# Optimization experiments

Hardware: AMD Instinct MI355X
Metric: run time of the kernel (lower is better)

## Reference

```python
import jax, jax.numpy as jnp
import numpy as np

N, L, V, H = 64, 2048, 32000, 512

def setup_inputs() -> dict:
    key = jax.random.key(0)
    ks = jax.random.split(key, 6)
    s = 1.0 / np.sqrt(H)
    return {
        "X": jax.random.randint(ks[0], (N, L), 0, V),
        "emb": jax.random.normal(ks[1], (V, H), jnp.float32),
        "W_hh": jax.random.normal(ks[2], (H, H), jnp.float32) * s,
        "b_hh": jax.random.normal(ks[3], (H,), jnp.float32) * s,
        "W_xh": jax.random.normal(ks[4], (H, H), jnp.float32) * s,
        "b_xh": jax.random.normal(ks[5], (H,), jnp.float32) * s,
    }

def reference(X, emb, W_hh, b_hh, W_xh, b_xh):
    # Embed all timesteps and apply the input projection once (batched GEMM);
    # identical math to per-step W_xh(E_t) + b_xh.
    E = emb[X]                                   # (N, L, H)
    Xh = jnp.einsum('nlh,kh->nlk', E, W_xh) + b_xh  # (N, L, H)

    def step(h, xh_t):
        # h_t = tanh(W_hh h_{t-1} + b_hh + W_xh x_t + b_xh)
        h = jnp.tanh(h @ W_hh.T + b_hh + xh_t)
        return h, h

    h0 = jnp.zeros((X.shape[0], W_hh.shape[0]), dtype=emb.dtype)
    _, H_all = jax.lax.scan(step, h0, jnp.swapaxes(Xh, 0, 1))  # (L, N, H)
    return jnp.swapaxes(H_all, 0, 1)             # (N, L, H)
```

## Files before the change

kernel.cpp:

```cpp
#include <hip/hip_runtime.h>


typedef _Float16 half8 __attribute__((ext_vector_type(8)));
typedef float    f32x4 __attribute__((ext_vector_type(4)));

#define MFMA_F16(A,B,C) __builtin_amdgcn_mfma_f32_16x16x32_f16(A,B,C,0,0,0)

static __device__ __forceinline__ half8 cvt8(const float* p){
  const f32x4* q = (const f32x4*)p;
  f32x4 a = q[0], b = q[1];
  half8 r;
  r[0]=(_Float16)a[0]; r[1]=(_Float16)a[1]; r[2]=(_Float16)a[2]; r[3]=(_Float16)a[3];
  r[4]=(_Float16)b[0]; r[5]=(_Float16)b[1]; r[6]=(_Float16)b[2]; r[7]=(_Float16)b[3];
  return r;
}

static __device__ __forceinline__ float tanh_fast(float z){
  float e = __expf(2.0f*z);
  return 1.0f - 2.0f/(e + 1.0f);
}

__global__ __launch_bounds__(256) void k_xh(
    const int* __restrict__ X, const float* __restrict__ emb,
    const float* __restrict__ Wxh, const float* __restrict__ bxh,
    const float* __restrict__ bhh, float* __restrict__ out)
{
  const int bid = blockIdx.x;
  const int bm = bid >> 3;
  const int bn = bid & 7;
  const int tid = threadIdx.x;
  const int w  = tid >> 6;
  const int l  = tid & 63;
  const int lr = l & 15, lq = l >> 4;

  const int mbase = bm*64 + (w>>1)*32;
  const int nbase = bn*64 + (w&1)*32;

  const int tok0 = X[mbase + lr];
  const int tok1 = X[mbase + 16 + lr];
  const int c0 = nbase + lr;
  const int c1 = nbase + 16 + lr;
  const float bs0 = bxh[c0] + bhh[c0];
  const float bs1 = bxh[c1] + bhh[c1];

  const float* a0 = emb + (long long)tok0*512 + lq*8;
  const float* a1 = emb + (long long)tok1*512 + lq*8;
  const float* b0 = Wxh + (long long)c0*512 + lq*8;
  const float* b1 = Wxh + (long long)c1*512 + lq*8;

  f32x4 acc00 = {0,0,0,0}, acc01 = {0,0,0,0}, acc10 = {0,0,0,0}, acc11 = {0,0,0,0};

  #pragma unroll
  for (int ks=0; ks<16; ++ks){
    half8 A0 = cvt8(a0 + ks*32);
    half8 A1 = cvt8(a1 + ks*32);
    half8 B0 = cvt8(b0 + ks*32);
    half8 B1 = cvt8(b1 + ks*32);
    acc00 = MFMA_F16(A0, B0, acc00);
    acc01 = MFMA_F16(A0, B1, acc01);
    acc10 = MFMA_F16(A1, B0, acc10);
    acc11 = MFMA_F16(A1, B1, acc11);
  }
  #pragma unroll
  for (int r=0; r<4; ++r){
    const long long m0 = mbase + 4*lq + r;
    const long long m1 = m0 + 16;
    out[m0*512 + c0] = acc00[r] + bs0;
    out[m0*512 + c1] = acc01[r] + bs1;
    out[m1*512 + c0] = acc10[r] + bs0;
    out[m1*512 + c1] = acc11[r] + bs1;
  }
}

__global__ __launch_bounds__(512, 2) void k_rnn(
    const float* __restrict__ Whh,
    float* out,
    unsigned long long* mb,
    unsigned int* flags)
{
  const int b = blockIdx.x;
  const int side    = (b>>3)&1;
  const int pair    = (b&7)*4 + (b>>4);
  const int partner = b ^ 8;
  const int tid = threadIdx.x;
  const int w = tid >> 6;
  const int l = tid & 63;
  const int lr = l & 15, lq = l >> 4;
  const int ln = l & 1;

  __shared__ _Float16 hl[2][2][264];

  for (int i = tid; i < 2*2*264; i += 512) (&hl[0][0][0])[i] = (_Float16)0.0f;

  const int cA = side*256 + w*32 + lr;
  const int cB = cA + 16;
  half8 WfA[16], WfB[16];
  #pragma unroll
  for (int ks=0; ks<8; ++ks){
    const int kown = (side*8 + ks)*32 + lq*8;
    const int kpar = ((side^1)*8 + ks)*32 + lq*8;
    WfA[ks]   = cvt8(Whh + (long long)cA*512 + kown);
    WfB[ks]   = cvt8(Whh + (long long)cB*512 + kown);
    WfA[8+ks] = cvt8(Whh + (long long)cA*512 + kpar);
    WfB[8+ks] = cvt8(Whh + (long long)cB*512 + kpar);
  }
  __syncthreads();

  const int n_row = pair*2 + ln;
  const long long row_base = (long long)n_row * 2048 * 512;
  const int ccol = side*256 + w*32 + lq*4;
  unsigned long long* mb_me = mb + (long long)b*256;
  unsigned long long* mb_pt = mb + (long long)partner*256;

  for (int t=0; t<2048; ++t){
    const int bufc = t & 1, bufp = bufc ^ 1;

    f32x4 xh0 = {0,0,0,0}, xh1 = {0,0,0,0};
    long long obase = 0;
    if (lr < 2){
      obase = row_base + (long long)t*512 + ccol;
      xh0 = *(const f32x4*)(out + obase);
      xh1 = *(const f32x4*)(out + obase + 16);
    }

    f32x4 acc0 = {0,0,0,0}, acc1 = {0,0,0,0};

    #pragma unroll
    for (int ks=0; ks<8; ++ks){
      half8 hf = *(const half8*)(&hl[bufp][ln][ks*32 + lq*8]);
      acc0 = MFMA_F16(WfA[ks], hf, acc0);
      acc1 = MFMA_F16(WfB[ks], hf, acc1);
    }

    if (t > 0){
      {
        int spin = 0;
        while (__hip_atomic_load(&flags[partner], __ATOMIC_RELAXED, __HIP_MEMORY_SCOPE_AGENT)
                 < (unsigned)t && ++spin < (1<<20)) {}
      }
      unsigned long long* mp = mb_pt + (long long)bufp*128 + ln*64;
      #pragma unroll
      for (int ks=0; ks<8; ++ks){
        const int ui = ks*8 + lq*2;
        unsigned long long u0 = __hip_atomic_load(&mp[ui],   __ATOMIC_RELAXED, __HIP_MEMORY_SCOPE_AGENT);
        unsigned long long u1 = __hip_atomic_load(&mp[ui+1], __ATOMIC_RELAXED, __HIP_MEMORY_SCOPE_AGENT);
        union { unsigned long long u[2]; half8 v; } cv;
        cv.u[0] = u0; cv.u[1] = u1;
        acc0 = MFMA_F16(WfA[8+ks], cv.v, acc0);
        acc1 = MFMA_F16(WfB[8+ks], cv.v, acc1);
      }
    }

    if (lr < 2){
      f32x4 h0, h1;
      #pragma unroll
      for (int r=0; r<4; ++r){
        h0[r] = tanh_fast(acc0[r] + xh0[r]);
        h1[r] = tanh_fast(acc1[r] + xh1[r]);
      }
      *(f32x4*)(out + obase)      = h0;
      *(f32x4*)(out + obase + 16) = h1;
      union { _Float16 h[4]; unsigned long long u; } p0, p1;
      #pragma unroll
      for (int r=0; r<4; ++r){ p0.h[r] = (_Float16)h0[r]; p1.h[r] = (_Float16)h1[r]; }
      const int cl = w*32 + lq*4;
      *(unsigned long long*)(&hl[bufc][ln][cl])      = p0.u;
      *(unsigned long long*)(&hl[bufc][ln][cl + 16]) = p1.u;
      unsigned long long* mm = mb_me + (long long)bufc*128 + ln*64;
      __hip_atomic_store(&mm[cl>>2],       p0.u, __ATOMIC_RELAXED, __HIP_MEMORY_SCOPE_AGENT);
      __hip_atomic_store(&mm[(cl>>2) + 4], p1.u, __ATOMIC_RELAXED, __HIP_MEMORY_SCOPE_AGENT);
    }

    __syncthreads();
    if (tid == 0)
      __hip_atomic_store(&flags[b], (unsigned)(t+1), __ATOMIC_RELAXED, __HIP_MEMORY_SCOPE_AGENT);
  }
}

extern "C" void kernel_launch(void* const* d_in, const int* in_sizes, int n_in,
                              void* d_out, int out_size, void* d_ws, size_t ws_size,
                              hipStream_t stream)
{
  const int*   X    = (const int*)  d_in[0];
  const float* emb  = (const float*)d_in[1];
  const float* Whh  = (const float*)d_in[2];
  const float* bhh  = (const float*)d_in[3];
  const float* Wxh  = (const float*)d_in[4];
  const float* bxh  = (const float*)d_in[5];
  float* out = (float*)d_out;

  unsigned long long* mb   = (unsigned long long*)d_ws;
  unsigned int*       flags = (unsigned int*)((char*)d_ws + 64*2048);

  hipMemsetAsync(flags, 0, 64*sizeof(unsigned int), stream);
  hipLaunchKernelGGL(k_xh,  dim3(16384), dim3(256), 0, stream, X, emb, Wxh, bxh, bhh, out);
  hipLaunchKernelGGL(k_rnn, dim3(64),    dim3(512), 0, stream, Whh, out, mb, flags);
}
```

Baseline: 8.174 ms.

## Keep whole W_hh per block, drop cross-block partner exchange in RNN

```diff
diff --git a/kernel.cpp b/kernel.cpp
--- a/kernel.cpp
+++ b/kernel.cpp
@@ -74,106 +74,93 @@
 
 __global__ __launch_bounds__(512, 2) void k_rnn(
     const float* __restrict__ Whh,
-    float* out,
-    unsigned long long* mb,
-    unsigned int* flags)
+    float* __restrict__ out)
 {
-  const int b = blockIdx.x;
-  const int side    = (b>>3)&1;
-  const int pair    = (b&7)*4 + (b>>4);
-  const int partner = b ^ 8;
+  const int b   = blockIdx.x;
   const int tid = threadIdx.x;
-  const int w = tid >> 6;
-  const int l = tid & 63;
-  const int lr = l & 15, lq = l >> 4;
-  const int ln = l & 1;
+  const int w   = tid >> 6;
+  const int l   = tid & 63;
+  const int lr  = l & 15;
+  const int kg  = l >> 4;
+  const int wc0 = w * 64;
 
-  __shared__ _Float16 hl[2][2][264];
+  __shared__ _Float16 wlds[8][16][512];
+  __shared__ _Float16 hbuf[2][2][520];
 
-  for (int i = tid; i < 2*2*264; i += 512) (&hl[0][0][0])[i] = (_Float16)0.0f;
+  for (int i = tid; i < 2*2*520; i += 512) (&hbuf[0][0][0])[i] = (_Float16)0.0f;
 
-  const int cA = side*256 + w*32 + lr;
-  const int cB = cA + 16;
-  half8 WfA[16], WfB[16];
+  half8 Wv[3][16];
   #pragma unroll
-  for (int ks=0; ks<8; ++ks){
-    const int kown = (side*8 + ks)*32 + lq*8;
-    const int kpar = ((side^1)*8 + ks)*32 + lq*8;
-    WfA[ks]   = cvt8(Whh + (long long)cA*512 + kown);
-    WfB[ks]   = cvt8(Whh + (long long)cB*512 + kown);
-    WfA[8+ks] = cvt8(Whh + (long long)cA*512 + kpar);
-    WfB[8+ks] = cvt8(Whh + (long long)cB*512 + kpar);
+  for (int ct = 0; ct < 3; ++ct){
+    #pragma unroll
+    for (int ks = 0; ks < 16; ++ks){
+      Wv[ct][ks] = cvt8(Whh + (long long)(wc0 + ct*16 + lr)*512 + ks*32 + kg*8);
+    }
+  }
+  #pragma unroll
+  for (int ks = 0; ks < 16; ++ks){
+    half8 v = cvt8(Whh + (long long)(wc0 + 48 + lr)*512 + ks*32 + kg*8);
+    *(half8*)&wlds[w][ks][l*8] = v;
   }
   __syncthreads();
 
-  const int n_row = pair*2 + ln;
-  const long long row_base = (long long)n_row * 2048 * 512;
-  const int ccol = side*256 + w*32 + lq*4;
-  unsigned long long* mb_me = mb + (long long)b*256;
-  unsigned long long* mb_pt = mb + (long long)partner*256;
+  const int jj = l & 1;
+  const long long nb = (long long)(b*2 + (lr < 2 ? lr : 0)) * 2048 * 512;
 
-  for (int t=0; t<2048; ++t){
+  for (int t = 0; t < 2048; ++t){
     const int bufc = t & 1, bufp = bufc ^ 1;
 
-    f32x4 xh0 = {0,0,0,0}, xh1 = {0,0,0,0};
-    long long obase = 0;
-    if (lr < 2){
-      obase = row_base + (long long)t*512 + ccol;
-      xh0 = *(const f32x4*)(out + obase);
-      xh1 = *(const f32x4*)(out + obase + 16);
+    f32x4 xh0 = {0,0,0,0}, xh1 = {0,0,0,0}, xh2 = {0,0,0,0}, xh3 = {0,0,0,0};
+    long long ob = 0;
+    const bool act = (lr < 2);
+    if (act){
+      ob = nb + (long long)t*512 + wc0 + kg*4;
+      xh0 = *(const f32x4*)(out + ob);
+      xh1 = *(const f32x4*)(out + ob + 16);
+      xh2 = *(const f32x4*)(out + ob + 32);
+      xh3 = *(const f32x4*)(out + ob + 48);
     }
 
-    f32x4 acc0 = {0,0,0,0}, acc1 = {0,0,0,0};
+    f32x4 acc0 = {0,0,0,0}, acc1 = {0,0,0,0}, acc2 = {0,0,0,0}, acc3 = {0,0,0,0};
 
     #pragma unroll
-    for (int ks=0; ks<8; ++ks){
-      half8 hf = *(const half8*)(&hl[bufp][ln][ks*32 + lq*8]);
-      acc0 = MFMA_F16(WfA[ks], hf, acc0);
-      acc1 = MFMA_F16(WfB[ks], hf, acc1);
+    for (int ks = 0; ks < 16; ++ks){
+      half8 hf = *(const half8*)&hbuf[bufp][jj][ks*32 + kg*8];
+      half8 w3 = *(const half8*)&wlds[w][ks][l*8];
+      acc0 = MFMA_F16(Wv[0][ks], hf, acc0);
+      acc1 = MFMA_F16(Wv[1][ks], hf, acc1);
+      acc2 = MFMA_F16(Wv[2][ks], hf, acc2);
+      acc3 = MFMA_F16(w3, hf, acc3);
     }
 
-    if (t > 0){
-      {
-        int spin = 0;
-        while (__hip_atomic_load(&flags[partner], __ATOMIC_RELAXED, __HIP_MEMORY_SCOPE_AGENT)
-                 < (unsigned)t && ++spin < (1<<20)) {}
-      }
-      unsigned long long* mp = mb_pt + (long long)bufp*128 + ln*64;
+    if (act){
+      f32x4 h0, h1, h2, h3;
       #pragma unroll
-      for (int ks=0; ks<8; ++ks){
-        const int ui = ks*8 + lq*2;
-        unsigned long long u0 = __hip_atomic_load(&mp[ui],   __ATOMIC_RELAXED, __HIP_MEMORY_SCOPE_AGENT);
-        unsigned long long u1 = __hip_atomic_load(&mp[ui+1], __ATOMIC_RELAXED, __HIP_MEMORY_SCOPE_AGENT);
-        union { unsigned long long u[2]; half8 v; } cv;
-        cv.u[0] = u0; cv.u[1] = u1;
-        acc0 = MFMA_F16(WfA[8+ks], cv.v, acc0);
-        acc1 = MFMA_F16(WfB[8+ks], cv.v, acc1);
-      }
-    }
-
-    if (lr < 2){
-      f32x4 h0, h1;
-      #pragma unroll
-      for (int r=0; r<4; ++r){
+      for (int r = 0; r < 4; ++r){
         h0[r] = tanh_fast(acc0[r] + xh0[r]);
         h1[r] = tanh_fast(acc1[r] + xh1[r]);
+        h2[r] = tanh_fast(acc2[r] + xh2[r]);
+        h3[r] = tanh_fast(acc3[r] + xh3[r]);
       }
-      *(f32x4*)(out + obase)      = h0;
-      *(f32x4*)(out + obase + 16) = h1;
-      union { _Float16 h[4]; unsigned long long u; } p0, p1;
+      *(f32x4*)(out + ob)      = h0;
+      *(f32x4*)(out + ob + 16) = h1;
+      *(f32x4*)(out + ob + 32) = h2;
+      *(f32x4*)(out + ob + 48) = h3;
+
+      union { _Float16 h[4]; unsigned long long u; } p0, p1, p2, p3;
       #pragma unroll
-      for (int r=0; r<4; ++r){ p0.h[r] = (_Float16)h0[r]; p1.h[r] = (_Float16)h1[r]; }
-      const int cl = w*32 + lq*4;
-      *(unsigned long long*)(&hl[bufc][ln][cl])      = p0.u;
-      *(unsigned long long*)(&hl[bufc][ln][cl + 16]) = p1.u;
-      unsigned long long* mm = mb_me + (long long)bufc*128 + ln*64;
-      __hip_atomic_store(&mm[cl>>2],       p0.u, __ATOMIC_RELAXED, __HIP_MEMORY_SCOPE_AGENT);
-      __hip_atomic_store(&mm[(cl>>2) + 4], p1.u, __ATOMIC_RELAXED, __HIP_MEMORY_SCOPE_AGENT);
+      for (int r = 0; r < 4; ++r){
+        p0.h[r] = (_Float16)h0[r]; p1.h[r] = (_Float16)h1[r];
+        p2.h[r] = (_Float16)h2[r]; p3.h[r] = (_Float16)h3[r];
+      }
+      const int cl = wc0 + kg*4;
+      *(unsigned long long*)&hbuf[bufc][lr][cl]      = p0.u;
+      *(unsigned long long*)&hbuf[bufc][lr][cl + 16] = p1.u;
+      *(unsigned long long*)&hbuf[bufc][lr][cl + 32] = p2.u;
+      *(unsigned long long*)&hbuf[bufc][lr][cl + 48] = p3.u;
     }
 
     __syncthreads();
-    if (tid == 0)
-      __hip_atomic_store(&flags[b], (unsigned)(t+1), __ATOMIC_RELAXED, __HIP_MEMORY_SCOPE_AGENT);
   }
 }
 
@@ -189,10 +176,6 @@
   const float* bxh  = (const float*)d_in[5];
   float* out = (float*)d_out;
 
-  unsigned long long* mb   = (unsigned long long*)d_ws;
-  unsigned int*       flags = (unsigned int*)((char*)d_ws + 64*2048);
-
-  hipMemsetAsync(flags, 0, 64*sizeof(unsigned int), stream);
   hipLaunchKernelGGL(k_xh,  dim3(16384), dim3(256), 0, stream, X, emb, Wxh, bxh, bhh, out);
-  hipLaunchKernelGGL(k_rnn, dim3(64),    dim3(512), 0, stream, Whh, out, mb, flags);
+  hipLaunchKernelGGL(k_rnn, dim3(32),    dim3(512), 0, stream, Whh, out);
 }
```

New measurement: 8.702 ms. 1.06x slower.
